# Kernel tuning notes

Hardware: AMD Instinct MI355X
Metric: run time of the kernel (lower is better)

## Reference

```python
import jax, jax.numpy as jnp
import numpy as np

B, N, IN_F = 4, 2048, 256
H, HEAD_DIM = 8, 32  # out_features=256, concat=True -> head_dim=32
ALPHA = 0.2
MASK_VAL = -9e15


def setup_inputs() -> dict:
    key = jax.random.key(0)
    k1, k2, k3, k4 = jax.random.split(key, 4)
    x = jax.random.normal(k1, (B, N, IN_F), dtype=jnp.float32)
    adj = jax.random.randint(k2, (B, N, N), 0, 2, dtype=jnp.int32)
    # xavier_uniform for W [H, in, head_dim]: gain=1, fan_in=in, fan_out=head_dim
    limW = float(np.sqrt(6.0 / (IN_F + HEAD_DIM)))
    W = jax.random.uniform(k3, (H, IN_F, HEAD_DIM), dtype=jnp.float32, minval=-limW, maxval=limW)
    # xavier_uniform for a [H, 2*head_dim]: fan_in=2*head_dim, fan_out=H (2D tensor)
    lima = float(np.sqrt(6.0 / (H + 2 * HEAD_DIM)))
    a = jax.random.uniform(k4, (H, 2 * HEAD_DIM), dtype=jnp.float32, minval=-lima, maxval=lima)
    return {"x": x, "adj": adj, "W": W, "a": a}


def reference(x, adj, W, a):
    # x: [B, N, F], adj: [B, N, N], W: [H, F, D], a: [H, 2D]
    D = W.shape[-1]
    Wh = jnp.einsum('bnf,hfd->bhnd', x, W)                     # [B,H,N,D]
    a_src, a_dst = a[:, :D], a[:, D:]
    # additive score e_ij = a_src . Wh_i + a_dst . Wh_j (equivalent to concat+matmul)
    e_i = jnp.einsum('bhnd,hd->bhn', Wh, a_src)                # [B,H,N]
    e_j = jnp.einsum('bhnd,hd->bhn', Wh, a_dst)                # [B,H,N]
    scores = e_i[:, :, :, None] + e_j[:, :, None, :]           # [B,H,N,N]
    scores = jnp.where(scores > 0, scores, ALPHA * scores)     # LeakyReLU
    scores = jnp.where(adj[:, None, :, :] == 0, MASK_VAL, scores)
    probs = jax.nn.softmax(scores, axis=-1)                    # [B,H,N,N]
    h = jnp.einsum('bhij,bhjd->bhid', probs, Wh)               # [B,H,N,D]
    b, n = x.shape[0], x.shape[1]
    return h.transpose(0, 2, 1, 3).reshape(b, n, h.shape[1] * D)  # concat heads
```

## Files before the change

### kernel.cpp

```cpp
#include <hip/hip_runtime.h>

#define BB 4
#define NN 2048
#define INF 256
#define HH 8
#define DD 32
#define LOG2E 1.4426950408889634f

typedef __attribute__((ext_vector_type(8))) short short8;
typedef __attribute__((ext_vector_type(4))) float f32x4;

__device__ __forceinline__ unsigned short bf16_rne(float v) {
    unsigned b = __float_as_uint(v);
    return (unsigned short)((b + 0x7fffu + ((b >> 16) & 1u)) >> 16);
}
__device__ __forceinline__ unsigned short bf16_rhu(float v) {
    return (unsigned short)((__float_as_uint(v) + 0x8000u) >> 16);
}

__global__ __launch_bounds__(256) void wprep_kernel(
    const float* __restrict__ W, const float* __restrict__ a,
    float* __restrict__ we_g, unsigned short* __restrict__ wT)
{
    const int bb = blockIdx.x, t = threadIdx.x;
    if (bb < 16) {
        const int h = bb & 7, sel = bb >> 3;
        const float* wr = W + ((size_t)(h * INF + t)) * DD;
        const float* av = a + h * 2 * DD + sel * DD;
        float acc = 0.f;
        #pragma unroll
        for (int d = 0; d < DD; ++d) acc += wr[d] * av[d];
        we_g[bb * INF + t] = acc * LOG2E;
    }
    #pragma unroll
    for (int r2 = 0; r2 < 8; ++r2) {
        int row = bb * 8 + r2;
        int h = row >> 5, d = row & 31;
        wT[row * INF + t] = bf16_rhu(W[((size_t)(h * INF + t)) * DD + d]);
    }
}

__global__ __launch_bounds__(256) void prebit_kernel(
    const int* __restrict__ adj, unsigned* __restrict__ bitsG)
{
    const int t = threadIdx.x, w = t >> 6, l = t & 63;
    const int sb = blockIdx.x * 256 + w * 64;
    #pragma unroll 1
    for (int i = 0; i < 16; ++i) {
        int s0 = sb + i * 4;
        int a0[4];
        #pragma unroll
        for (int u = 0; u < 4; ++u) {
            int s = s0 + u;
            a0[u] = adj[((size_t)(s >> 5)) * 2048 + (s & 31) * 64 + l];
        }
        #pragma unroll
        for (int u = 0; u < 4; ++u) {
            int s = s0 + u;
            unsigned long long m = __ballot(a0[u] != 0);
            if (l == 0)
                *(uint2*)&bitsG[((size_t)(s >> 5)) * 64 + (s & 31) * 2] =
                    make_uint2((unsigned)m, (unsigned)(m >> 32));
        }
    }
}

__global__ __launch_bounds__(256) void ek_kernel(
    const float* __restrict__ x, const float* __restrict__ we_g,
    float* __restrict__ esrc, unsigned* __restrict__ ejP)
{
    __shared__ __align__(16) float xs[16 * 260];
    __shared__ __align__(16) float weld2[16 * 260];
    const int t = threadIdx.x;
    const int tile = blockIdx.x & 127, b = blockIdx.x >> 7;
    const int n0 = tile * 16;

    #pragma unroll
    for (int p = 0; p < 4; ++p) {
        int flat = p * 1024 + t * 4;
        int row = flat >> 8, col = flat & 255;
        f32x4 g = *(const f32x4*)&x[((size_t)(b * NN + n0 + row)) * INF + col];
        *(f32x4*)&xs[row * 260 + col] = g;
    }
    #pragma unroll
    for (int p = 0; p < 4; ++p) {
        int flat = p * 1024 + t * 4;
        f32x4 g = *(const f32x4*)&we_g[flat];
        int f = flat & 255;
        *(f32x4*)&weld2[(f >> 4) * 260 + (flat >> 8) * 16 + (f & 15)] = g;
    }
    __syncthreads();

    const int row = t >> 4, c = t & 15;
    f32x4 xv[4];
    #pragma unroll
    for (int i = 0; i < 4; ++i)
        xv[i] = *(const f32x4*)&xs[row * 260 + c * 16 + i * 4];

    float keep = 0.f;
    #pragma unroll
    for (int k = 0; k < 16; ++k) {
        float s = 0.f;
        #pragma unroll
        for (int i = 0; i < 4; ++i) {
            f32x4 w4 = *(const f32x4*)&weld2[c * 260 + k * 16 + i * 4];
            s += xv[i][0]*w4[0] + xv[i][1]*w4[1] + xv[i][2]*w4[2] + xv[i][3]*w4[3];
        }
        s += __shfl_xor(s, 1, 64);
        s += __shfl_xor(s, 2, 64);
        s += __shfl_xor(s, 4, 64);
        s += __shfl_xor(s, 8, 64);
        keep = (c == k) ? s : keep;
    }
    const int n = n0 + row;
    if (c < 8) {
        esrc[(b * 8 + c) * NN + n] = keep;
    } else {
        float Ej  = __builtin_amdgcn_exp2f(keep);
        float Ej5 = __builtin_amdgcn_exp2f(0.2f * keep);
        ejP[(b * 8 + (c - 8)) * NN + n] =
            ((unsigned)bf16_rne(Ej) << 16) | (unsigned)bf16_rne(Ej5);
    }
}

__global__ __launch_bounds__(256) void whk_kernel(
    const float* __restrict__ x, const unsigned short* __restrict__ wT,
    unsigned short* __restrict__ whT2)
{
    __shared__ __align__(16) unsigned short xb[64 * 264];
    __shared__ __align__(16) unsigned short wb[64 * 264];
    const int t = threadIdx.x;
    const int hp = blockIdx.x & 3, tl = (blockIdx.x >> 2) & 31, b = blockIdx.x >> 7;
    const int n0 = tl * 64;

    #pragma unroll
    for (int p = 0; p < 16; ++p) {
        int flat = p * 1024 + t * 4;
        int row = flat >> 8, col = flat & 255;
        f32x4 g = *(const f32x4*)&x[((size_t)(b * NN + n0 + row)) * INF + col];
        unsigned a0 = __float_as_uint(g[0]) + 0x8000u;
        unsigned a1 = __float_as_uint(g[1]) + 0x8000u;
        unsigned a2 = __float_as_uint(g[2]) + 0x8000u;
        unsigned a3 = __float_as_uint(g[3]) + 0x8000u;
        uint2 pk;
        pk.x = __builtin_amdgcn_perm(a1, a0, 0x07060302u);
        pk.y = __builtin_amdgcn_perm(a3, a2, 0x07060302u);
        *(uint2*)&xb[row * 264 + col] = pk;
    }
    #pragma unroll
    for (int p = 0; p < 8; ++p) {
        int flat = p * 2048 + t * 8;
        int cc = flat >> 8, f = flat & 255;
        *(short8*)&wb[cc * 264 + f] = *(const short8*)&wT[(hp * 64 + cc) * INF + f];
    }
    __syncthreads();

    const int w = t >> 6, l = t & 63;
    const int ml = l & 15, q = l >> 4;
    f32x4 acc[4] = {};
    const unsigned short* ap = &xb[(w * 16 + ml) * 264 + q * 8];
    #pragma unroll
    for (int k0 = 0; k0 < INF; k0 += 32) {
        short8 A = *(const short8*)&ap[k0];
        #pragma unroll
        for (int c16 = 0; c16 < 4; ++c16) {
            short8 Bf = *(const short8*)&wb[(c16 * 16 + ml) * 264 + q * 8 + k0];
            acc[c16] = __builtin_amdgcn_mfma_f32_16x16x32_bf16(A, Bf, acc[c16], 0, 0, 0);
        }
    }
    __syncthreads();

    unsigned short* ldsC = xb;
    #pragma unroll
    for (int c16 = 0; c16 < 4; ++c16)
        #pragma unroll
        for (int r = 0; r < 4; ++r) {
            int col = c16 * 16 + ml;
            int rt  = w * 16 + q * 4 + r;
            ldsC[col * 72 + rt] = bf16_rhu(acc[c16][r]);
        }
    __syncthreads();

    #pragma unroll
    for (int p = 0; p < 2; ++p) {
        int g = p * 256 + t;
        int d = g & 31, jo = (g >> 5) & 7, h2 = g >> 8;
        short8 vv = *(const short8*)&ldsC[(h2 * 32 + d) * 72 + jo * 8];
        int bh = b * 8 + hp * 2 + h2;
        *(short8*)&whT2[(((size_t)bh * 256 + tl * 8 + jo) * 32 + d) * 8] = vv;
    }
}

__global__ __launch_bounds__(1024, 4) void attn_kernel(
    const unsigned* __restrict__ bitsG, const unsigned short* __restrict__ whT2,
    const float* __restrict__ esrc, const unsigned* __restrict__ ejP,
    float* __restrict__ out)
{
    __shared__ __align__(16) float cmb[8][64][25];
    const int t = threadIdx.x, v = t >> 6, l = t & 63;
    const int h = v & 7, js = v >> 3;
    const int ml = l & 15, q = l >> 4;
    const int it = blockIdx.x & 63, b = blockIdx.x >> 6;
    const int i0 = it * 32;
    const int bh = b * HH + h;

    const float ei0 = esrc[bh * NN + i0 + ml];
    const float ei1 = esrc[bh * NN + i0 + 16 + ml];
    const float Ei0  = __builtin_amdgcn_exp2f(ei0);
    const float Ei05 = __builtin_amdgcn_exp2f(0.2f * ei0);
    const float Ei1  = __builtin_amdgcn_exp2f(ei1);
    const float Ei15 = __builtin_amdgcn_exp2f(0.2f * ei1);

    const unsigned* epP = ejP + bh * NN + js * 1024;
    const unsigned short* whb = whT2 + ((size_t)bh * 256 + js * 128) * 256;
    const unsigned* bg0 = bitsG + ((size_t)(b * NN + i0 + ml)) * 64 + js * 32;
    const unsigned* bg1 = bitsG + ((size_t)(b * NN + i0 + 16 + ml)) * 64 + js * 32;

    const short8 ones = {0x3F80, 0x3F80, 0x3F80, 0x3F80, 0x3F80, 0x3F80, 0x3F80, 0x3F80};
    f32x4 acc00 = {}, acc01 = {}, acc10 = {}, acc11 = {}, accD0 = {}, accD1 = {};

    #pragma unroll 2
    for (int c = 0; c < 8; ++c) {
        unsigned w0a[4], w1a[4];
        *(uint4*)w0a = *(const uint4*)&bg0[c * 4];
        *(uint4*)w1a = *(const uint4*)&bg1[c * 4];
        const unsigned* epc = epP + c * 128;
        #pragma unroll
        for (int k = 0; k < 4; ++k) {
            const int jb = k * 32 + q * 8;
            uint4 epA = *(const uint4*)&epc[jb];
            uint4 epB = *(const uint4*)&epc[jb + 4];
            const unsigned short* wp = whb + (size_t)(c * 16 + k * 4 + q) * 256;
            short8 B0 = *(const short8*)&wp[ml * 8];
            short8 B1 = *(const short8*)&wp[(16 + ml) * 8];
            unsigned st0 = w0a[k] >> (q * 8);
            unsigned st1 = w1a[k] >> (q * 8);
            union { unsigned u[4]; short8 s; } f0, f1;
            const unsigned* ea = &epA.x;
            const unsigned* eb = &epB.x;
            #pragma unroll
            for (int pp = 0; pp < 4; ++pp) {
                unsigned pkA = (pp < 2) ? ea[2 * pp]     : eb[2 * pp - 4];
                unsigned pkB = (pp < 2) ? ea[2 * pp + 1] : eb[2 * pp - 3];
                float EjA = __uint_as_float(pkA & 0xffff0000u);
                float FjA = __uint_as_float(pkA << 16);
                float EjB = __uint_as_float(pkB & 0xffff0000u);
                float FjB = __uint_as_float(pkB << 16);
                unsigned mA0 = (unsigned)__builtin_amdgcn_sbfe(st0, 2 * pp, 1);
                unsigned mB0 = (unsigned)__builtin_amdgcn_sbfe(st0, 2 * pp + 1, 1);
                unsigned mA1 = (unsigned)__builtin_amdgcn_sbfe(st1, 2 * pp, 1);
                unsigned mB1 = (unsigned)__builtin_amdgcn_sbfe(st1, 2 * pp + 1, 1);
                float pA0 = fmaxf(EjA * Ei0, FjA * Ei05);
                float pB0 = fmaxf(EjB * Ei0, FjB * Ei05);
                float pA1 = fmaxf(EjA * Ei1, FjA * Ei15);
                float pB1 = fmaxf(EjB * Ei1, FjB * Ei15);
                f0.u[pp] = __builtin_amdgcn_perm(__float_as_uint(pB0) & mB0,
                                                 __float_as_uint(pA0) & mA0,
                                                 0x07060302u);
                f1.u[pp] = __builtin_amdgcn_perm(__float_as_uint(pB1) & mB1,
                                                 __float_as_uint(pA1) & mA1,
                                                 0x07060302u);
            }
            acc00 = __builtin_amdgcn_mfma_f32_16x16x32_bf16(f0.s, B0, acc00, 0, 0, 0);
            acc01 = __builtin_amdgcn_mfma_f32_16x16x32_bf16(f0.s, B1, acc01, 0, 0, 0);
            accD0 = __builtin_amdgcn_mfma_f32_16x16x32_bf16(f0.s, ones, accD0, 0, 0, 0);
            acc10 = __builtin_amdgcn_mfma_f32_16x16x32_bf16(f1.s, B0, acc10, 0, 0, 0);
            acc11 = __builtin_amdgcn_mfma_f32_16x16x32_bf16(f1.s, B1, acc11, 0, 0, 0);
            accD1 = __builtin_amdgcn_mfma_f32_16x16x32_bf16(f1.s, ones, accD1, 0, 0, 0);
        }
    }

    float* myc = &cmb[h][l][0];
    if (js == 1) {
        *(f32x4*)&myc[0]  = acc00; *(f32x4*)&myc[4]  = acc01;
        *(f32x4*)&myc[8]  = acc10; *(f32x4*)&myc[12] = acc11;
        *(f32x4*)&myc[16] = accD0; *(f32x4*)&myc[20] = accD1;
    }
    __syncthreads();
    if (js == 0) {
        f32x4 o00 = *(const f32x4*)&myc[0],  o01 = *(const f32x4*)&myc[4];
        f32x4 o10 = *(const f32x4*)&myc[8],  o11 = *(const f32x4*)&myc[12];
        f32x4 oD0 = *(const f32x4*)&myc[16], oD1 = *(const f32x4*)&myc[20];
        #pragma unroll
        for (int r = 0; r < 4; ++r) {
            int ir0 = i0 + q * 4 + r;
            int ir1 = i0 + 16 + q * 4 + r;
            float inv0 = 1.0f / (accD0[r] + oD0[r]);
            float inv1 = 1.0f / (accD1[r] + oD1[r]);
            size_t ba0 = ((size_t)(b * NN + ir0)) * (HH * DD) + h * DD;
            size_t ba1 = ((size_t)(b * NN + ir1)) * (HH * DD) + h * DD;
            out[ba0 + ml]      = (acc00[r] + o00[r]) * inv0;
            out[ba0 + 16 + ml] = (acc01[r] + o01[r]) * inv0;
            out[ba1 + ml]      = (acc10[r] + o10[r]) * inv1;
            out[ba1 + 16 + ml] = (acc11[r] + o11[r]) * inv1;
        }
    }
}

extern "C" void kernel_launch(void* const* d_in, const int* in_sizes, int n_in,
                              void* d_out, int out_size, void* d_ws, size_t ws_size,
                              hipStream_t stream) {
    (void)in_sizes; (void)n_in; (void)out_size; (void)ws_size;
    const float* x   = (const float*)d_in[0];
    const int*   adj = (const int*)d_in[1];
    const float* W   = (const float*)d_in[2];
    const float* a   = (const float*)d_in[3];
    float* out = (float*)d_out;

    char* ws = (char*)d_ws;
    unsigned short* whT2 = (unsigned short*)ws;
    unsigned short* wT   = (unsigned short*)(ws + (4u << 20));
    float*    esrc = (float*)(ws + (4u << 20) + (128u << 10));
    unsigned* ejP  = (unsigned*)(esrc + BB * HH * NN);
    float*    we_g = (float*)(ejP + BB * HH * NN);
    unsigned* bitsG = (unsigned*)(we_g + 16 * INF);

    wprep_kernel <<<dim3(32),   dim3(256),  0, stream>>>(W, a, we_g, wT);
    prebit_kernel<<<dim3(1024), dim3(256),  0, stream>>>(adj, bitsG);
    ek_kernel    <<<dim3(512),  dim3(256),  0, stream>>>(x, we_g, esrc, ejP);
    whk_kernel   <<<dim3(512),  dim3(256),  0, stream>>>(x, wT, whT2);
    attn_kernel  <<<dim3(256),  dim3(1024), 0, stream>>>(bitsG, whT2, esrc, ejP, out);
}
```

Baseline: 166.4 us.

## Halve attention row tile, double grid, and fold source exponent into one factor

Each attention block now handles 16 query rows instead of 32, the grid doubles to 512 blocks, and launch bounds ask for higher occupancy. The per-row exp(e_i) factor is divided out of the softmax numerator and denominator, leaving a single multiply by exp2(-0.8*e_i) in the inner loop. This cuts per-thread registers and VALU work and spreads blocks across more waves. In exchange, each block gets half the reuse of the loaded Wh tiles and ej values, so L2 traffic rises, and the rescaling changes bf16 rounding of the probabilities.

```diff
diff --git a/kernel.cpp b/kernel.cpp
--- a/kernel.cpp
+++ b/kernel.cpp
@@ -191,39 +191,33 @@
     }
 }
 
-__global__ __launch_bounds__(1024, 4) void attn_kernel(
+__global__ __launch_bounds__(1024, 8) void attn_kernel(
     const unsigned* __restrict__ bitsG, const unsigned short* __restrict__ whT2,
     const float* __restrict__ esrc, const unsigned* __restrict__ ejP,
     float* __restrict__ out)
 {
-    __shared__ __align__(16) float cmb[8][64][25];
+    __shared__ __align__(16) float cmb[8][64][13];
     const int t = threadIdx.x, v = t >> 6, l = t & 63;
     const int h = v & 7, js = v >> 3;
     const int ml = l & 15, q = l >> 4;
-    const int it = blockIdx.x & 63, b = blockIdx.x >> 6;
-    const int i0 = it * 32;
+    const int it = blockIdx.x & 127, b = blockIdx.x >> 7;
+    const int i0 = it * 16;
     const int bh = b * HH + h;
 
-    const float ei0 = esrc[bh * NN + i0 + ml];
-    const float ei1 = esrc[bh * NN + i0 + 16 + ml];
-    const float Ei0  = __builtin_amdgcn_exp2f(ei0);
-    const float Ei05 = __builtin_amdgcn_exp2f(0.2f * ei0);
-    const float Ei1  = __builtin_amdgcn_exp2f(ei1);
-    const float Ei15 = __builtin_amdgcn_exp2f(0.2f * ei1);
+    const float ei = esrc[bh * NN + i0 + ml];
+    const float ri = __builtin_amdgcn_exp2f(-0.8f * ei);
 
     const unsigned* epP = ejP + bh * NN + js * 1024;
     const unsigned short* whb = whT2 + ((size_t)bh * 256 + js * 128) * 256;
     const unsigned* bg0 = bitsG + ((size_t)(b * NN + i0 + ml)) * 64 + js * 32;
-    const unsigned* bg1 = bitsG + ((size_t)(b * NN + i0 + 16 + ml)) * 64 + js * 32;
 
     const short8 ones = {0x3F80, 0x3F80, 0x3F80, 0x3F80, 0x3F80, 0x3F80, 0x3F80, 0x3F80};
-    f32x4 acc00 = {}, acc01 = {}, acc10 = {}, acc11 = {}, accD0 = {}, accD1 = {};
+    f32x4 acc0 = {}, acc1 = {}, accD = {};
 
     #pragma unroll 2
     for (int c = 0; c < 8; ++c) {
-        unsigned w0a[4], w1a[4];
-        *(uint4*)w0a = *(const uint4*)&bg0[c * 4];
-        *(uint4*)w1a = *(const uint4*)&bg1[c * 4];
+        unsigned wa[4];
+        *(uint4*)wa = *(const uint4*)&bg0[c * 4];
         const unsigned* epc = epP + c * 128;
         #pragma unroll
         for (int k = 0; k < 4; ++k) {
@@ -233,9 +227,8 @@
             const unsigned short* wp = whb + (size_t)(c * 16 + k * 4 + q) * 256;
             short8 B0 = *(const short8*)&wp[ml * 8];
             short8 B1 = *(const short8*)&wp[(16 + ml) * 8];
-            unsigned st0 = w0a[k] >> (q * 8);
-            unsigned st1 = w1a[k] >> (q * 8);
-            union { unsigned u[4]; short8 s; } f0, f1;
+            unsigned st = wa[k] >> (q * 8);
+            union { unsigned u[4]; short8 s; } f0;
             const unsigned* ea = &epA.x;
             const unsigned* eb = &epB.x;
             #pragma unroll
@@ -246,53 +239,38 @@
                 float FjA = __uint_as_float(pkA << 16);
                 float EjB = __uint_as_float(pkB & 0xffff0000u);
                 float FjB = __uint_as_float(pkB << 16);
-                unsigned mA0 = (unsigned)__builtin_amdgcn_sbfe(st0, 2 * pp, 1);
-                unsigned mB0 = (unsigned)__builtin_amdgcn_sbfe(st0, 2 * pp + 1, 1);
-                unsigned mA1 = (unsigned)__builtin_amdgcn_sbfe(st1, 2 * pp, 1);
-                unsigned mB1 = (unsigned)__builtin_amdgcn_sbfe(st1, 2 * pp + 1, 1);
-                float pA0 = fmaxf(EjA * Ei0, FjA * Ei05);
-                float pB0 = fmaxf(EjB * Ei0, FjB * Ei05);
-                float pA1 = fmaxf(EjA * Ei1, FjA * Ei15);
-                float pB1 = fmaxf(EjB * Ei1, FjB * Ei15);
-                f0.u[pp] = __builtin_amdgcn_perm(__float_as_uint(pB0) & mB0,
-                                                 __float_as_uint(pA0) & mA0,
-                                                 0x07060302u);
-                f1.u[pp] = __builtin_amdgcn_perm(__float_as_uint(pB1) & mB1,
-                                                 __float_as_uint(pA1) & mA1,
+                unsigned mA = (unsigned)__builtin_amdgcn_sbfe(st, 2 * pp, 1);
+                unsigned mB = (unsigned)__builtin_amdgcn_sbfe(st, 2 * pp + 1, 1);
+                float pA = fmaxf(EjA, FjA * ri);
+                float pB = fmaxf(EjB, FjB * ri);
+                f0.u[pp] = __builtin_amdgcn_perm(__float_as_uint(pB) & mB,
+                                                 __float_as_uint(pA) & mA,
                                                  0x07060302u);
             }
-            acc00 = __builtin_amdgcn_mfma_f32_16x16x32_bf16(f0.s, B0, acc00, 0, 0, 0);
-            acc01 = __builtin_amdgcn_mfma_f32_16x16x32_bf16(f0.s, B1, acc01, 0, 0, 0);
-            accD0 = __builtin_amdgcn_mfma_f32_16x16x32_bf16(f0.s, ones, accD0, 0, 0, 0);
-            acc10 = __builtin_amdgcn_mfma_f32_16x16x32_bf16(f1.s, B0, acc10, 0, 0, 0);
-            acc11 = __builtin_amdgcn_mfma_f32_16x16x32_bf16(f1.s, B1, acc11, 0, 0, 0);
-            accD1 = __builtin_amdgcn_mfma_f32_16x16x32_bf16(f1.s, ones, accD1, 0, 0, 0);
+            acc0 = __builtin_amdgcn_mfma_f32_16x16x32_bf16(f0.s, B0, acc0, 0, 0, 0);
+            acc1 = __builtin_amdgcn_mfma_f32_16x16x32_bf16(f0.s, B1, acc1, 0, 0, 0);
+            accD = __builtin_amdgcn_mfma_f32_16x16x32_bf16(f0.s, ones, accD, 0, 0, 0);
         }
     }
 
     float* myc = &cmb[h][l][0];
     if (js == 1) {
-        *(f32x4*)&myc[0]  = acc00; *(f32x4*)&myc[4]  = acc01;
-        *(f32x4*)&myc[8]  = acc10; *(f32x4*)&myc[12] = acc11;
-        *(f32x4*)&myc[16] = accD0; *(f32x4*)&myc[20] = accD1;
+        *(f32x4*)&myc[0] = acc0;
+        *(f32x4*)&myc[4] = acc1;
+        *(f32x4*)&myc[8] = accD;
     }
     __syncthreads();
     if (js == 0) {
-        f32x4 o00 = *(const f32x4*)&myc[0],  o01 = *(const f32x4*)&myc[4];
-        f32x4 o10 = *(const f32x4*)&myc[8],  o11 = *(const f32x4*)&myc[12];
-        f32x4 oD0 = *(const f32x4*)&myc[16], oD1 = *(const f32x4*)&myc[20];
+        f32x4 o0 = *(const f32x4*)&myc[0];
+        f32x4 o1 = *(const f32x4*)&myc[4];
+        f32x4 oD = *(const f32x4*)&myc[8];
         #pragma unroll
         for (int r = 0; r < 4; ++r) {
-            int ir0 = i0 + q * 4 + r;
-            int ir1 = i0 + 16 + q * 4 + r;
-            float inv0 = 1.0f / (accD0[r] + oD0[r]);
-            float inv1 = 1.0f / (accD1[r] + oD1[r]);
-            size_t ba0 = ((size_t)(b * NN + ir0)) * (HH * DD) + h * DD;
-            size_t ba1 = ((size_t)(b * NN + ir1)) * (HH * DD) + h * DD;
-            out[ba0 + ml]      = (acc00[r] + o00[r]) * inv0;
-            out[ba0 + 16 + ml] = (acc01[r] + o01[r]) * inv0;
-            out[ba1 + ml]      = (acc10[r] + o10[r]) * inv1;
-            out[ba1 + 16 + ml] = (acc11[r] + o11[r]) * inv1;
+            int ir = i0 + q * 4 + r;
+            float inv = 1.0f / (accD[r] + oD[r]);
+            size_t ba = ((size_t)(b * NN + ir)) * (HH * DD) + h * DD;
+            out[ba + ml]      = (acc0[r] + o0[r]) * inv;
+            out[ba + 16 + ml] = (acc1[r] + o1[r]) * inv;
         }
     }
 }
@@ -319,5 +297,5 @@
     prebit_kernel<<<dim3(1024), dim3(256),  0, stream>>>(adj, bitsG);
     ek_kernel    <<<dim3(512),  dim3(256),  0, stream>>>(x, we_g, esrc, ejP);
     whk_kernel   <<<dim3(512),  dim3(256),  0, stream>>>(x, wT, whT2);
-    attn_kernel  <<<dim3(256),  dim3(1024), 0, stream>>>(bitsG, whT2, esrc, ejP, out);
-}
+    attn_kernel  <<<dim3(512),  dim3(1024), 0, stream>>>(bitsG, whT2, esrc, ejP, out);
+}
```

Result: slower. 171.1 us (+2.8%).
